# Performance work log

Hardware: AMD Instinct MI355X
Metric: run time of the kernel (lower is better)

The kernel has to match this reference:

```python
import jax, jax.numpy as jnp
import numpy as np


def _cell(x, h, c, Wih, Whh, bih, bhh):
    # PyTorch LSTMCell: gates = x@Wih^T + bih + h@Whh^T + bhh, gate order i,f,g,o
    g = x @ Wih.T + bih + h @ Whh.T + bhh
    i, f, gg, o = jnp.split(g, 4, axis=-1)
    c_new = jax.nn.sigmoid(f) * c + jax.nn.sigmoid(i) * jnp.tanh(gg)
    h_new = jax.nn.sigmoid(o) * jnp.tanh(c_new)
    return h_new, c_new


def _forward(input, covariates, W_ih0, W_hh0, b_ih0, b_hh0,
             W_ih_r, W_hh_r, b_ih_r, b_hh_r, Wl, bl, future):
    B, T, _ = input.shape
    H = W_hh0.shape[1]
    Lm1 = W_ih_r.shape[0]  # number of stacked cells after layer 0

    # conditioning inputs: concat series with covariates -> [T, B, input_dim]
    xs = jnp.swapaxes(jnp.concatenate([input, covariates[:, :T, :]], axis=2), 0, 1)

    h0 = jnp.zeros((B, H), input.dtype)
    c0 = jnp.zeros((B, H), input.dtype)
    hr = jnp.zeros((Lm1, B, H), input.dtype)
    cr = jnp.zeros((Lm1, B, H), input.dtype)

    def run(state, x_t):
        h0, c0, hr, cr = state
        h0, c0 = _cell(x_t, h0, c0, W_ih0, W_hh0, b_ih0, b_hh0)
        prev = h0
        hs, cs = [], []
        for n in range(Lm1):  # static small loop over layers
            hn, cn = _cell(prev, hr[n], cr[n], W_ih_r[n], W_hh_r[n], b_ih_r[n], b_hh_r[n])
            hs.append(hn); cs.append(cn)
            prev = hn
        out = prev @ Wl.T + bl  # [B, output_dim]
        return (h0, c0, jnp.stack(hs), jnp.stack(cs)), out

    state, outs_cond = jax.lax.scan(run, (h0, c0, hr, cr), xs)  # outs_cond: [T,B,out]

    if future > 0:
        cov_f = jnp.swapaxes(covariates[:, T:T + future, :], 0, 1)  # [F,B,cov]

        def fut(carry, cov_t):
            state, out = carry
            x_t = jnp.concatenate([out, cov_t], axis=1)
            state, out = run(state, x_t)
            return (state, out), out

        _, outs_fut = jax.lax.scan(fut, (state, outs_cond[-1]), cov_f)
        outs = jnp.concatenate([outs_cond, outs_fut], axis=0)
    else:
        outs = outs_cond
    return jnp.swapaxes(outs, 0, 1)  # [B, T+future, output_dim]


def setup_inputs() -> dict:
    key = jax.random.key(0)
    ks = jax.random.split(key, 12)
    B, T, F = 512, 256, 64
    H, IN, COV, OUT, L = 1024, 8, 7, 1, 4
    s = 0.05
    return {
        "input": jax.random.normal(ks[0], (B, T, OUT), dtype=jnp.float32),
        "covariates": jax.random.normal(ks[1], (B, T + F, COV), dtype=jnp.float32),
        "W_ih0": jax.random.normal(ks[2], (4 * H, IN), dtype=jnp.float32) * s,
        "W_hh0": jax.random.normal(ks[3], (4 * H, H), dtype=jnp.float32) * s,
        "b_ih0": jax.random.normal(ks[4], (4 * H,), dtype=jnp.float32) * s,
        "b_hh0": jax.random.normal(ks[5], (4 * H,), dtype=jnp.float32) * s,
        "W_ih_r": jax.random.normal(ks[6], (L - 1, 4 * H, H), dtype=jnp.float32) * s,
        "W_hh_r": jax.random.normal(ks[7], (L - 1, 4 * H, H), dtype=jnp.float32) * s,
        "b_ih_r": jax.random.normal(ks[8], (L - 1, 4 * H), dtype=jnp.float32) * s,
        "b_hh_r": jax.random.normal(ks[9], (L - 1, 4 * H), dtype=jnp.float32) * s,
        "Wl": jax.random.normal(ks[10], (OUT, H), dtype=jnp.float32) * s,
        "bl": jax.random.normal(ks[11], (OUT,), dtype=jnp.float32) * s,
        "future": F,
    }


def reference(input, covariates, W_ih0, W_hh0, b_ih0, b_hh0,
              W_ih_r, W_hh_r, b_ih_r, b_hh_r, Wl, bl, future):
    return _forward(input, covariates, W_ih0, W_hh0, b_ih0, b_hh0,
                    W_ih_r, W_hh_r, b_ih_r, b_hh_r, Wl, bl, future)
```

## Files before the change

### kernel.cpp

```cpp
#include <hip/hip_runtime.h>

typedef _Float16 f16;
typedef __attribute__((ext_vector_type(8))) _Float16 half8;
typedef __attribute__((ext_vector_type(4))) float f32x4;
typedef __attribute__((ext_vector_type(4))) unsigned int uint4v;

#define B_   512
#define T_   256
#define TT_  320
#define KB0  33
#define KBR  64
#define NSLOT 12

struct PP {
  const f16* Wt[4];
  f16* xh[4][2];
  float* cst;
  const float* bias;
  const float* input;
  const float* cov;
  const float* Wl;
  const float* blp;
  float* out;
};

__device__ __forceinline__ void gload16(const void* g, void* l) {
  __builtin_amdgcn_global_load_lds((const __attribute__((address_space(1))) void*)g,
                                   (__attribute__((address_space(3))) void*)l,
                                   16, 0, 0);
}

__device__ __forceinline__ float sigf(float x) {
  return __builtin_amdgcn_rcpf(1.f + __builtin_amdgcn_exp2f(-1.44269504f * x));
}
__device__ __forceinline__ float tanhf_(float x) {
  return 2.f * __builtin_amdgcn_rcpf(1.f + __builtin_amdgcn_exp2f(-2.88539008f * x)) - 1.f;
}

__device__ __forceinline__ int haddr(int k, int m) {
  return (k >> 5) * 16384 + (m >> 4) * 512 + ((m & 15) + ((k & 31) >> 3) * 16) * 8 + (k & 7);
}

#define WAITBAR(vm) asm volatile("s_waitcnt vmcnt(" #vm ") lgkmcnt(0)\n\ts_barrier" ::: "memory")

__global__ __launch_bounds__(256, 2) void lstm_diag2(PP P, int d)
{
  __shared__ f16 lds_a[4][4096];
  __shared__ f16 lds_b[4][4096];
  const int tid = threadIdx.x;
  const int ln = tid & 63, w = tid >> 6;
  const int mg = w >> 1, np = w & 1;
  const int bid = blockIdx.x;
  const int xcd = bid & 7;
  const int j   = bid >> 3;
  const int l   = j & 3;
  const int k   = j >> 2;
  const int mb  = k & 3;
  const int nb  = xcd + 8 * (k >> 2);
  const int m0  = mb * 128;
  const int t = d - l;
  if (t < 0 || t >= T_) return;

  const int p = t & 1, q = p ^ 1;
  const f16* __restrict__ Wt = P.Wt[l];
  const int KB   = (l == 0) ? KB0 : KBR;
  const int koff = (l == 0) ? 32 : 1024;
  const f16* __restrict__ src = P.xh[l][p];
  f16* __restrict__ selfd     = P.xh[l][q];
  f16* __restrict__ nextd     = (l < 3) ? P.xh[l + 1][p] : nullptr;
  const float* __restrict__ bias4 = P.bias + l * 4096;
  float* __restrict__ cst = P.cst + (size_t)l * 524288;

  if (l == 0 && nb == 0 && tid < 128) P.out[(size_t)(m0 + tid) * TT_ + t] = P.blp[0];

  auto stageA = [&](int slot, int kb) {
    const f16* g0 = src + (size_t)kb * 16384 + mb * 4096;
    gload16(g0 + tid * 8,         &lds_a[slot][tid * 8]);
    gload16(g0 + (tid + 256) * 8, &lds_a[slot][(tid + 256) * 8]);
  };
  auto stageB = [&](int slot, int kb) {
    #pragma unroll
    for (int jj = 0; jj < 2; ++jj) {
      const int e = tid + jj * 256;
      const int panel = e >> 8, rem = e & 255;
      gload16(Wt + ((size_t)((nb * 2 + panel) * KB + kb)) * 2048 + rem * 8,
              &lds_b[slot][e * 8]);
    }
  };
  auto genA0 = [&]() {
    #pragma unroll
    for (int jj = 0; jj < 2; ++jj) {
      const int idx = tid + jj * 256;
      const int lx = idx & 63, mf = idx >> 6, r = lx & 15, kgrp = lx >> 4;
      const int brow = m0 + mf * 16 + r;
      half8 v;
      #pragma unroll
      for (int z = 0; z < 8; ++z) v[z] = (f16)0.f;
      if (kgrp == 0) {
        v[0] = (f16)P.input[brow * T_ + t];
        const float* cp = P.cov + ((size_t)brow * TT_ + t) * 7;
        #pragma unroll
        for (int z = 1; z < 8; ++z) v[z] = (f16)cp[z - 1];
      }
      *(half8*)&lds_a[0][idx * 8] = v;
    }
  };

  f32x4 acc[4][4];
  #pragma unroll
  for (int m = 0; m < 4; ++m)
    #pragma unroll
    for (int g = 0; g < 4; ++g) { acc[m][g][0]=0.f; acc[m][g][1]=0.f; acc[m][g][2]=0.f; acc[m][g][3]=0.f; }

  if (l == 0) {
    genA0();
    stageB(0, 0);
    stageA(1, 1); stageB(1, 1);
    stageA(2, 2); stageB(2, 2);
  } else {
    stageA(0, 0); stageB(0, 0);
    stageA(1, 1); stageB(1, 1);
    stageA(2, 2); stageB(2, 2);
  }

  for (int i = 0; i < KB; ++i) {
    WAITBAR(8);
    const int slot = i & 3;
    const half8* A  = (const half8*)&lds_a[slot][0];
    const half8* Bp = (const half8*)&lds_b[slot][0];
    half8 a[4], b[4];
    #pragma unroll
    for (int m = 0; m < 4; ++m) a[m] = A[(mg * 4 + m) * 64 + ln];
    #pragma unroll
    for (int g = 0; g < 4; ++g) b[g] = Bp[(np * 4 + g) * 64 + ln];
    int kn = i + 3; if (kn >= KB) kn = KB - 1;
    stageA((i + 3) & 3, kn); stageB((i + 3) & 3, kn);
    __builtin_amdgcn_s_setprio(1);
    #pragma unroll
    for (int m = 0; m < 4; ++m)
      #pragma unroll
      for (int g = 0; g < 4; ++g)
        acc[m][g] = __builtin_amdgcn_mfma_f32_16x16x32_f16(a[m], b[g], acc[m][g], 0, 0, 0);
    __builtin_amdgcn_s_setprio(0);
  }
  WAITBAR(0);

  const int col = (nb * 2 + np) * 16 + (ln & 15);
  const float bi  = bias4[col];
  const float bff = bias4[1024 + col];
  const float bgg = bias4[2048 + col];
  const float bo  = bias4[3072 + col];
  const float wl  = (l == 3) ? P.Wl[col] : 0.f;
  #pragma unroll
  for (int m = 0; m < 4; ++m) {
    const int rowb = m0 + (mg * 4 + m) * 16 + (ln >> 4) * 4;
    #pragma unroll
    for (int r = 0; r < 4; ++r) {
      const int row = rowb + r;
      float gi = acc[m][0][r] + bi;
      float gf = acc[m][1][r] + bff;
      float gg = acc[m][2][r] + bgg;
      float go = acc[m][3][r] + bo;
      float* cp = cst + (size_t)row * 1024 + col;
      float cn = sigf(gf) * (*cp) + sigf(gi) * tanhf_(gg);
      float h  = sigf(go) * tanhf_(cn);
      *cp = cn;
      f16 hh = (f16)h;
      selfd[haddr(koff + col, row)] = hh;
      if (l < 3) {
        nextd[haddr(col, row)] = hh;
      } else {
        float val = h * wl;
        val += __shfl_xor(val, 1);
        val += __shfl_xor(val, 2);
        val += __shfl_xor(val, 4);
        val += __shfl_xor(val, 8);
        if ((ln & 15) == 0) atomicAdd(P.out + (size_t)row * TT_ + t, val);
      }
    }
  }
}

__global__ __launch_bounds__(512) void lstm_cells(PP P, int d, int lbeg, int lend, int tlim)
{
  __shared__ f16 lds[NSLOT][6144];
  const int tid = threadIdx.x;
  const int ln = tid & 63, w = tid >> 6;
  const int mg = w & 1, kg = w >> 1;
  const int nb = blockIdx.x & 63, mb = blockIdx.x >> 6;
  const int m0 = mb * 128, n0 = nb * 16;

  for (int l = lbeg; l <= lend; ++l) {
    const int t = d - l;
    if (t < 0 || t >= tlim) continue;

    const int p = t & 1, q = p ^ 1;
    const f16* __restrict__ Wt = P.Wt[l];
    const int KB   = (l == 0) ? KB0 : KBR;
    const int mode = (l == 0) ? 0 : ((l == 3) ? 2 : 1);
    const int koff = (l == 0) ? 32 : 1024;
    const f16* __restrict__ src   = P.xh[l][p];
    f16* __restrict__ selfd       = P.xh[l][q];
    f16* __restrict__ nextd       = (l < 3) ? P.xh[l + 1][p] : nullptr;
    const float* __restrict__ bias4 = P.bias + l * 4096;
    float* __restrict__ cst = P.cst + (size_t)l * 524288;

    if (mode == 0 && nb == 0 && tid < 128) P.out[(size_t)(m0 + tid) * TT_ + t] = P.blp[0];

    auto stage_slab = [&](int slot, int kb) {
      if (mode == 0 && kb == 0) {
        int mf = tid >> 6, r = ln & 15, kgrp = ln >> 4;
        int brow = m0 + mf * 16 + r;
        half8 v;
        #pragma unroll
        for (int jj = 0; jj < 8; ++jj) v[jj] = (f16)0.f;
        if (kgrp == 0) {
          float x0 = (t < T_) ? P.input[brow * T_ + t] : P.out[(size_t)brow * TT_ + (t - 1)];
          v[0] = (f16)x0;
          const float* cp = P.cov + ((size_t)brow * TT_ + t) * 7;
          #pragma unroll
          for (int jj = 1; jj < 8; ++jj) v[jj] = (f16)cp[jj - 1];
        }
        *(half8*)&lds[slot][tid * 8] = v;
      } else {
        gload16(src + (size_t)kb * 16384 + mb * 4096 + tid * 8, &lds[slot][tid * 8]);
      }
      if (tid < 256)
        gload16(Wt + ((size_t)(nb * KB + kb)) * 2048 + tid * 8, &lds[slot][4096 + tid * 8]);
    };
    auto stage_round = [&](int r) {
      int base = (r % 3) * 4;
      #pragma unroll
      for (int jj = 0; jj < 4; ++jj) {
        int kb = r * 4 + jj;
        if (kb >= KB) kb = KB - 1;
        stage_slab(base + jj, kb);
      }
    };

    f32x4 acc[4][4];
    #pragma unroll
    for (int m = 0; m < 4; ++m)
      #pragma unroll
      for (int g = 0; g < 4; ++g) { acc[m][g][0]=0.f; acc[m][g][1]=0.f; acc[m][g][2]=0.f; acc[m][g][3]=0.f; }

    const int R = (KB + 3) >> 2;
    stage_round(0); stage_round(1);
    for (int i = 0; i < R; ++i) {
      if (i < R - 1) { if (w < 4) WAITBAR(8); else WAITBAR(4); }
      else           { WAITBAR(0); }
      const int kb = i * 4 + kg;
      const int slot = (i % 3) * 4 + kg;
      const half8* A  = (const half8*)&lds[slot][0];
      const half8* Bp = (const half8*)&lds[slot][4096];
      const bool live = (kb < KB);
      half8 a0, a1, a2, a3, b0, b1, b2, b3;
      if (live) {
        a0 = A[(mg * 4 + 0) * 64 + ln];
        a1 = A[(mg * 4 + 1) * 64 + ln];
        a2 = A[(mg * 4 + 2) * 64 + ln];
        a3 = A[(mg * 4 + 3) * 64 + ln];
        b0 = Bp[ln]; b1 = Bp[64 + ln]; b2 = Bp[128 + ln]; b3 = Bp[192 + ln];
      }
      if (i + 2 < R) stage_round(i + 2);
      if (live) {
        acc[0][0] = __builtin_amdgcn_mfma_f32_16x16x32_f16(a0, b0, acc[0][0], 0, 0, 0);
        acc[0][1] = __builtin_amdgcn_mfma_f32_16x16x32_f16(a0, b1, acc[0][1], 0, 0, 0);
        acc[0][2] = __builtin_amdgcn_mfma_f32_16x16x32_f16(a0, b2, acc[0][2], 0, 0, 0);
        acc[0][3] = __builtin_amdgcn_mfma_f32_16x16x32_f16(a0, b3, acc[0][3], 0, 0, 0);
        acc[1][0] = __builtin_amdgcn_mfma_f32_16x16x32_f16(a1, b0, acc[1][0], 0, 0, 0);
        acc[1][1] = __builtin_amdgcn_mfma_f32_16x16x32_f16(a1, b1, acc[1][1], 0, 0, 0);
        acc[1][2] = __builtin_amdgcn_mfma_f32_16x16x32_f16(a1, b2, acc[1][2], 0, 0, 0);
        acc[1][3] = __builtin_amdgcn_mfma_f32_16x16x32_f16(a1, b3, acc[1][3], 0, 0, 0);
        acc[2][0] = __builtin_amdgcn_mfma_f32_16x16x32_f16(a2, b0, acc[2][0], 0, 0, 0);
        acc[2][1] = __builtin_amdgcn_mfma_f32_16x16x32_f16(a2, b1, acc[2][1], 0, 0, 0);
        acc[2][2] = __builtin_amdgcn_mfma_f32_16x16x32_f16(a2, b2, acc[2][2], 0, 0, 0);
        acc[2][3] = __builtin_amdgcn_mfma_f32_16x16x32_f16(a2, b3, acc[2][3], 0, 0, 0);
        acc[3][0] = __builtin_amdgcn_mfma_f32_16x16x32_f16(a3, b0, acc[3][0], 0, 0, 0);
        acc[3][1] = __builtin_amdgcn_mfma_f32_16x16x32_f16(a3, b1, acc[3][1], 0, 0, 0);
        acc[3][2] = __builtin_amdgcn_mfma_f32_16x16x32_f16(a3, b2, acc[3][2], 0, 0, 0);
        acc[3][3] = __builtin_amdgcn_mfma_f32_16x16x32_f16(a3, b3, acc[3][3], 0, 0, 0);
      }
    }

    __syncthreads();
    float* red = (float*)&lds[0][0];
    #pragma unroll
    for (int m = 0; m < 4; ++m)
      #pragma unroll
      for (int g = 0; g < 4; ++g)
        *(f32x4*)&red[w * 4096 + (m * 4 + g) * 256 + ln * 4] = acc[m][g];
    __syncthreads();
    f32x4 facc[4];
    #pragma unroll
    for (int g = 0; g < 4; ++g) { facc[g][0]=0.f; facc[g][1]=0.f; facc[g][2]=0.f; facc[g][3]=0.f; }
    const int mgw = w >> 2, mlw = w & 3;
    #pragma unroll
    for (int kg2 = 0; kg2 < 4; ++kg2) {
      const int wsrc = kg2 * 2 + mgw;
      #pragma unroll
      for (int g = 0; g < 4; ++g) {
        f32x4 pv = *(const f32x4*)&red[wsrc * 4096 + (mlw * 4 + g) * 256 + ln * 4];
        facc[g][0] += pv[0]; facc[g][1] += pv[1]; facc[g][2] += pv[2]; facc[g][3] += pv[3];
      }
    }
    __syncthreads();

    const int col = n0 + (ln & 15);
    const int rowb = m0 + w * 16 + (ln >> 4) * 4;
    const float bi  = bias4[col];
    const float bff = bias4[1024 + col];
    const float bgg = bias4[2048 + col];
    const float bo  = bias4[3072 + col];
    const float wl  = (mode == 2) ? P.Wl[col] : 0.f;
    #pragma unroll
    for (int r = 0; r < 4; ++r) {
      const int row = rowb + r;
      float gi = facc[0][r] + bi;
      float gf = facc[1][r] + bff;
      float gg = facc[2][r] + bgg;
      float go = facc[3][r] + bo;
      float* cp = cst + (size_t)row * 1024 + col;
      float cn = sigf(gf) * (*cp) + sigf(gi) * tanhf_(gg);
      float h  = sigf(go) * tanhf_(cn);
      *cp = cn;
      f16 hh = (f16)h;
      selfd[haddr(koff + col, row)] = hh;
      if (mode != 2) {
        nextd[haddr(col, row)] = hh;
      } else {
        float val = h * wl;
        val += __shfl_xor(val, 1);
        val += __shfl_xor(val, 2);
        val += __shfl_xor(val, 4);
        val += __shfl_xor(val, 8);
        if ((ln & 15) == 0) atomicAdd(P.out + (size_t)row * TT_ + t, val);
      }
    }
  }
}

__global__ void zero_ws(uint4v* pz, int n)
{
  int i = blockIdx.x * 256 + threadIdx.x;
  if (i < n) { uint4v z; z[0] = 0u; z[1] = 0u; z[2] = 0u; z[3] = 0u; pz[i] = z; }
}

__global__ void pack_weights(const float* __restrict__ Wih0, const float* __restrict__ Whh0,
                             const float* __restrict__ Wihr, const float* __restrict__ Whhr,
                             f16* __restrict__ Wt0, f16* __restrict__ Wt1,
                             f16* __restrict__ Wt2, f16* __restrict__ Wt3)
{
  const int layer = blockIdx.y;
  const size_t e = (size_t)blockIdx.x * 256 + threadIdx.x;
  const int KB = layer ? KBR : KB0;
  if (e >= (size_t)64 * KB * 2048) return;
  const int panel = (int)(e >> 11), win = (int)(e & 2047);
  const int g = win >> 9, lane = (win >> 3) & 63, j = win & 7;
  const int nb = panel / KB, kb = panel - nb * KB;
  const int n = nb * 16 + (lane & 15);
  const int k = kb * 32 + (lane >> 4) * 8 + j;
  const int jr = g * 1024 + n;
  float v;
  if (layer == 0) {
    if (k < 8)       v = Wih0[jr * 8 + k];
    else if (k < 32) v = 0.f;
    else             v = Whh0[(size_t)jr * 1024 + (k - 32)];
  } else {
    const size_t base = (size_t)(layer - 1) * 4096 * 1024 + (size_t)jr * 1024;
    v = (k < 1024) ? Wihr[base + k] : Whhr[base + (k - 1024)];
  }
  f16 hv = (f16)v;
  if      (layer == 0) Wt0[e] = hv;
  else if (layer == 1) Wt1[e] = hv;
  else if (layer == 2) Wt2[e] = hv;
  else                 Wt3[e] = hv;
}

__global__ void pack_bias(const float* __restrict__ bih0, const float* __restrict__ bhh0,
                          const float* __restrict__ bihr, const float* __restrict__ bhhr,
                          float* __restrict__ bias)
{
  const int idx = blockIdx.x * 256 + threadIdx.x;
  const int lyr = idx >> 12, j = idx & 4095;
  bias[idx] = (lyr == 0) ? (bih0[j] + bhh0[j])
                         : (bihr[(lyr - 1) * 4096 + j] + bhhr[(lyr - 1) * 4096 + j]);
}

extern "C" void kernel_launch(void* const* d_in, const int* in_sizes, int n_in,
                              void* d_out, int out_size, void* d_ws, size_t ws_size,
                              hipStream_t stream)
{
  const float* input = (const float*)d_in[0];
  const float* cov   = (const float*)d_in[1];
  const float* Wih0  = (const float*)d_in[2];
  const float* Whh0  = (const float*)d_in[3];
  const float* bih0  = (const float*)d_in[4];
  const float* bhh0  = (const float*)d_in[5];
  const float* Wihr  = (const float*)d_in[6];
  const float* Whhr  = (const float*)d_in[7];
  const float* bihr  = (const float*)d_in[8];
  const float* bhhr  = (const float*)d_in[9];
  const float* Wl    = (const float*)d_in[10];
  const float* blp   = (const float*)d_in[11];
  float* out = (float*)d_out;
  char* ws = (char*)d_ws;

  const size_t XH0 = 1081344, XHR = 2097152;
  PP Pv;
  Pv.xh[0][0] = (f16*)(ws);            Pv.xh[0][1] = (f16*)(ws + XH0);
  Pv.xh[1][0] = (f16*)(ws + 2162688);  Pv.xh[1][1] = (f16*)(ws + 2162688 + XHR);
  Pv.xh[2][0] = (f16*)(ws + 6356992);  Pv.xh[2][1] = (f16*)(ws + 6356992 + XHR);
  Pv.xh[3][0] = (f16*)(ws + 10551296); Pv.xh[3][1] = (f16*)(ws + 10551296 + XHR);
  Pv.cst     = (float*)(ws + 14745600);
  float* bias = (float*)(ws + 23134208);
  f16* Wt0 = (f16*)(ws + 23199744);
  f16* Wt1 = (f16*)(ws + 31850496);
  f16* Wt2 = (f16*)(ws + 48627712);
  f16* Wt3 = (f16*)(ws + 65404928);
  Pv.Wt[0] = Wt0; Pv.Wt[1] = Wt1; Pv.Wt[2] = Wt2; Pv.Wt[3] = Wt3;
  Pv.bias = bias; Pv.input = input; Pv.cov = cov;
  Pv.Wl = Wl; Pv.blp = blp; Pv.out = out;

  pack_weights<<<dim3(32768, 4), 256, 0, stream>>>(Wih0, Whh0, Wihr, Whhr, Wt0, Wt1, Wt2, Wt3);
  pack_bias<<<64, 256, 0, stream>>>(bih0, bhh0, bihr, bhhr, bias);
  zero_ws<<<5648, 256, 0, stream>>>((uint4v*)ws, 23134208 / 16);

  for (int dg = 0; dg <= 258; ++dg)
    lstm_diag2<<<512, 256, 0, stream>>>(Pv, dg);
  for (int t = T_; t < TT_; ++t)
    for (int l = 0; l < 4; ++l)
      lstm_cells<<<256, 512, 0, stream>>>(Pv, t + l, l, l, TT_);
}
```

Before: 14.96 ms.

## Load weight fragments directly to registers and deepen activation LDS pipeline

The diagonal wavefront kernel stops staging weight tiles through LDS. Each wave now loads its B fragments straight from global memory into registers, two k-blocks ahead, using even/odd register sets. The freed LDS holds an 8-slot activation ring with 7-deep prefetch, and blocks are remapped so each layer lands on a fixed XCD pair. The intent is to cut LDS traffic and barrier pressure for weights and hide more latency, at the cost of register pressure, uncoalesced-ish global loads per wave and padded dummy rounds when KB is not a multiple of 8.

New measurement: 16.67 ms. +11.4%, slower.

```diff
diff --git a/kernel.cpp b/kernel.cpp
--- a/kernel.cpp
+++ b/kernel.cpp
@@ -42,22 +42,22 @@
 }
 
 #define WAITBAR(vm) asm volatile("s_waitcnt vmcnt(" #vm ") lgkmcnt(0)\n\ts_barrier" ::: "memory")
-
-__global__ __launch_bounds__(256, 2) void lstm_diag2(PP P, int d)
-{
-  __shared__ f16 lds_a[4][4096];
-  __shared__ f16 lds_b[4][4096];
+#define FENCE asm volatile("" ::: "memory")
+#define MFMA16(a, b, c) __builtin_amdgcn_mfma_f32_16x16x32_f16(a, b, c, 0, 0, 0)
+
+__global__ __launch_bounds__(256, 2) void lstm_diag3(PP P, int d)
+{
+  __shared__ f16 lds_a[8][4096];
   const int tid = threadIdx.x;
   const int ln = tid & 63, w = tid >> 6;
   const int mg = w >> 1, np = w & 1;
   const int bid = blockIdx.x;
-  const int xcd = bid & 7;
-  const int j   = bid >> 3;
-  const int l   = j & 3;
-  const int k   = j >> 2;
-  const int mb  = k & 3;
-  const int nb  = xcd + 8 * (k >> 2);
-  const int m0  = mb * 128;
+  const int l    = (bid & 7) >> 1;
+  const int nbhi = bid & 1;
+  const int rest = bid >> 3;
+  const int mb   = rest & 3;
+  const int nb   = nbhi * 16 + (rest >> 2);
+  const int m0   = mb * 128;
   const int t = d - l;
   if (t < 0 || t >= T_) return;
 
@@ -73,19 +73,12 @@
 
   if (l == 0 && nb == 0 && tid < 128) P.out[(size_t)(m0 + tid) * TT_ + t] = P.blp[0];
 
+  const f16* wb = Wt + ((size_t)(nb * 2 + np) * KB) * 2048 + ln * 8;
+
   auto stageA = [&](int slot, int kb) {
     const f16* g0 = src + (size_t)kb * 16384 + mb * 4096;
     gload16(g0 + tid * 8,         &lds_a[slot][tid * 8]);
     gload16(g0 + (tid + 256) * 8, &lds_a[slot][(tid + 256) * 8]);
-  };
-  auto stageB = [&](int slot, int kb) {
-    #pragma unroll
-    for (int jj = 0; jj < 2; ++jj) {
-      const int e = tid + jj * 256;
-      const int panel = e >> 8, rem = e & 255;
-      gload16(Wt + ((size_t)((nb * 2 + panel) * KB + kb)) * 2048 + rem * 8,
-              &lds_b[slot][e * 8]);
-    }
   };
   auto genA0 = [&]() {
     #pragma unroll
@@ -112,37 +105,68 @@
     #pragma unroll
     for (int g = 0; g < 4; ++g) { acc[m][g][0]=0.f; acc[m][g][1]=0.f; acc[m][g][2]=0.f; acc[m][g][3]=0.f; }
 
-  if (l == 0) {
-    genA0();
-    stageB(0, 0);
-    stageA(1, 1); stageB(1, 1);
-    stageA(2, 2); stageB(2, 2);
-  } else {
-    stageA(0, 0); stageB(0, 0);
-    stageA(1, 1); stageB(1, 1);
-    stageA(2, 2); stageB(2, 2);
+  if (l == 0) genA0(); else { stageA(0, 0); FENCE; }
+  stageA(1, 1); FENCE; stageA(2, 2); FENCE; stageA(3, 3); FENCE;
+  stageA(4, 4); FENCE; stageA(5, 5); FENCE; stageA(6, 6); FENCE;
+  half8 bE0 = *(const half8*)(wb);
+  half8 bE1 = *(const half8*)(wb + 512);
+  half8 bE2 = *(const half8*)(wb + 1024);
+  half8 bE3 = *(const half8*)(wb + 1536);
+  half8 bO0 = *(const half8*)(wb + 2048);
+  half8 bO1 = *(const half8*)(wb + 2560);
+  half8 bO2 = *(const half8*)(wb + 3072);
+  half8 bO3 = *(const half8*)(wb + 3584);
+
+#define RND(r, Bq0, Bq1, Bq2, Bq3)                                              \
+  { const int i = g8 + (r);                                                     \
+    WAITBAR(20);                                                                \
+    const half8* A = (const half8*)&lds_a[(r)][0];                              \
+    half8 a0 = A[(mg * 4 + 0) * 64 + ln];                                       \
+    half8 a1 = A[(mg * 4 + 1) * 64 + ln];                                       \
+    half8 a2 = A[(mg * 4 + 2) * 64 + ln];                                       \
+    half8 a3 = A[(mg * 4 + 3) * 64 + ln];                                       \
+    int ka = i + 7; if (ka >= KB) ka = KB - 1;                                  \
+    stageA(((r) + 7) & 7, ka);                                                  \
+    int kp = i + 2; if (kp >= KB) kp = KB - 1;                                  \
+    const f16* bp = wb + (size_t)kp * 2048;                                     \
+    half8 n0 = *(const half8*)(bp);                                             \
+    half8 n1 = *(const half8*)(bp + 512);                                       \
+    half8 n2 = *(const half8*)(bp + 1024);                                      \
+    half8 n3 = *(const half8*)(bp + 1536);                                      \
+    if (i < KB) {                                                               \
+      __builtin_amdgcn_s_setprio(1);                                            \
+      acc[0][0] = MFMA16(a0, Bq0, acc[0][0]);                                   \
+      acc[0][1] = MFMA16(a0, Bq1, acc[0][1]);                                   \
+      acc[0][2] = MFMA16(a0, Bq2, acc[0][2]);                                   \
+      acc[0][3] = MFMA16(a0, Bq3, acc[0][3]);                                   \
+      acc[1][0] = MFMA16(a1, Bq0, acc[1][0]);                                   \
+      acc[1][1] = MFMA16(a1, Bq1, acc[1][1]);                                   \
+      acc[1][2] = MFMA16(a1, Bq2, acc[1][2]);                                   \
+      acc[1][3] = MFMA16(a1, Bq3, acc[1][3]);                                   \
+      acc[2][0] = MFMA16(a2, Bq0, acc[2][0]);                                   \
+      acc[2][1] = MFMA16(a2, Bq1, acc[2][1]);                                   \
+      acc[2][2] = MFMA16(a2, Bq2, acc[2][2]);                                   \
+      acc[2][3] = MFMA16(a2, Bq3, acc[2][3]);                                   \
+      acc[3][0] = MFMA16(a3, Bq0, acc[3][0]);                                   \
+      acc[3][1] = MFMA16(a3, Bq1, acc[3][1]);                                   \
+      acc[3][2] = MFMA16(a3, Bq2, acc[3][2]);                                   \
+      acc[3][3] = MFMA16(a3, Bq3, acc[3][3]);                                   \
+      __builtin_amdgcn_s_setprio(0);                                            \
+    }                                                                           \
+    Bq0 = n0; Bq1 = n1; Bq2 = n2; Bq3 = n3; }
+
+  const int KBpad = (KB + 7) & ~7;
+  for (int g8 = 0; g8 < KBpad; g8 += 8) {
+    RND(0, bE0, bE1, bE2, bE3)
+    RND(1, bO0, bO1, bO2, bO3)
+    RND(2, bE0, bE1, bE2, bE3)
+    RND(3, bO0, bO1, bO2, bO3)
+    RND(4, bE0, bE1, bE2, bE3)
+    RND(5, bO0, bO1, bO2, bO3)
+    RND(6, bE0, bE1, bE2, bE3)
+    RND(7, bO0, bO1, bO2, bO3)
   }
-
-  for (int i = 0; i < KB; ++i) {
-    WAITBAR(8);
-    const int slot = i & 3;
-    const half8* A  = (const half8*)&lds_a[slot][0];
-    const half8* Bp = (const half8*)&lds_b[slot][0];
-    half8 a[4], b[4];
-    #pragma unroll
-    for (int m = 0; m < 4; ++m) a[m] = A[(mg * 4 + m) * 64 + ln];
-    #pragma unroll
-    for (int g = 0; g < 4; ++g) b[g] = Bp[(np * 4 + g) * 64 + ln];
-    int kn = i + 3; if (kn >= KB) kn = KB - 1;
-    stageA((i + 3) & 3, kn); stageB((i + 3) & 3, kn);
-    __builtin_amdgcn_s_setprio(1);
-    #pragma unroll
-    for (int m = 0; m < 4; ++m)
-      #pragma unroll
-      for (int g = 0; g < 4; ++g)
-        acc[m][g] = __builtin_amdgcn_mfma_f32_16x16x32_f16(a[m], b[g], acc[m][g], 0, 0, 0);
-    __builtin_amdgcn_s_setprio(0);
-  }
+#undef RND
   WAITBAR(0);
 
   const int col = (nb * 2 + np) * 16 + (ln & 15);
@@ -264,22 +288,22 @@
       }
       if (i + 2 < R) stage_round(i + 2);
       if (live) {
-        acc[0][0] = __builtin_amdgcn_mfma_f32_16x16x32_f16(a0, b0, acc[0][0], 0, 0, 0);
-        acc[0][1] = __builtin_amdgcn_mfma_f32_16x16x32_f16(a0, b1, acc[0][1], 0, 0, 0);
-        acc[0][2] = __builtin_amdgcn_mfma_f32_16x16x32_f16(a0, b2, acc[0][2], 0, 0, 0);
-        acc[0][3] = __builtin_amdgcn_mfma_f32_16x16x32_f16(a0, b3, acc[0][3], 0, 0, 0);
-        acc[1][0] = __builtin_amdgcn_mfma_f32_16x16x32_f16(a1, b0, acc[1][0], 0, 0, 0);
-        acc[1][1] = __builtin_amdgcn_mfma_f32_16x16x32_f16(a1, b1, acc[1][1], 0, 0, 0);
-        acc[1][2] = __builtin_amdgcn_mfma_f32_16x16x32_f16(a1, b2, acc[1][2], 0, 0, 0);
-        acc[1][3] = __builtin_amdgcn_mfma_f32_16x16x32_f16(a1, b3, acc[1][3], 0, 0, 0);
-        acc[2][0] = __builtin_amdgcn_mfma_f32_16x16x32_f16(a2, b0, acc[2][0], 0, 0, 0);
-        acc[2][1] = __builtin_amdgcn_mfma_f32_16x16x32_f16(a2, b1, acc[2][1], 0, 0, 0);
-        acc[2][2] = __builtin_amdgcn_mfma_f32_16x16x32_f16(a2, b2, acc[2][2], 0, 0, 0);
-        acc[2][3] = __builtin_amdgcn_mfma_f32_16x16x32_f16(a2, b3, acc[2][3], 0, 0, 0);
-        acc[3][0] = __builtin_amdgcn_mfma_f32_16x16x32_f16(a3, b0, acc[3][0], 0, 0, 0);
-        acc[3][1] = __builtin_amdgcn_mfma_f32_16x16x32_f16(a3, b1, acc[3][1], 0, 0, 0);
-        acc[3][2] = __builtin_amdgcn_mfma_f32_16x16x32_f16(a3, b2, acc[3][2], 0, 0, 0);
-        acc[3][3] = __builtin_amdgcn_mfma_f32_16x16x32_f16(a3, b3, acc[3][3], 0, 0, 0);
+        acc[0][0] = MFMA16(a0, b0, acc[0][0]);
+        acc[0][1] = MFMA16(a0, b1, acc[0][1]);
+        acc[0][2] = MFMA16(a0, b2, acc[0][2]);
+        acc[0][3] = MFMA16(a0, b3, acc[0][3]);
+        acc[1][0] = MFMA16(a1, b0, acc[1][0]);
+        acc[1][1] = MFMA16(a1, b1, acc[1][1]);
+        acc[1][2] = MFMA16(a1, b2, acc[1][2]);
+        acc[1][3] = MFMA16(a1, b3, acc[1][3]);
+        acc[2][0] = MFMA16(a2, b0, acc[2][0]);
+        acc[2][1] = MFMA16(a2, b1, acc[2][1]);
+        acc[2][2] = MFMA16(a2, b2, acc[2][2]);
+        acc[2][3] = MFMA16(a2, b3, acc[2][3]);
+        acc[3][0] = MFMA16(a3, b0, acc[3][0]);
+        acc[3][1] = MFMA16(a3, b1, acc[3][1]);
+        acc[3][2] = MFMA16(a3, b2, acc[3][2]);
+        acc[3][3] = MFMA16(a3, b3, acc[3][3]);
       }
     }
 
@@ -427,7 +451,7 @@
   zero_ws<<<5648, 256, 0, stream>>>((uint4v*)ws, 23134208 / 16);
 
   for (int dg = 0; dg <= 258; ++dg)
-    lstm_diag2<<<512, 256, 0, stream>>>(Pv, dg);
+    lstm_diag3<<<512, 256, 0, stream>>>(Pv, dg);
   for (int t = T_; t < TT_; ++t)
     for (int l = 0; l < 4; ++l)
       lstm_cells<<<256, 512, 0, stream>>>(Pv, t + l, l, l, TT_);
```
